# Kernel optimization log

Hardware: AMD Instinct MI355X
Metric: run time of the kernel (lower is better)

## Reference

```python
import jax, jax.numpy as jnp
import numpy as np

N_HEAD = 16
N_KV_HEAD = 4
HEAD_DIM = 128  # n_embd // n_head = 2048 // 16


def _apply_rope(x, pos, T):
    # x: [B, H, T, D]; RoPE cache built exactly like the torch module:
    # cos/sin use repeat_interleave(2) on freqs, rotation uses half-split.
    D = x.shape[-1]
    half = D // 2
    inv_freq = 1.0 / jnp.power(10000.0, jnp.arange(0, D, 2, dtype=jnp.float32) / D)  # [half]
    t = jnp.arange(pos, pos + T, dtype=jnp.float32)                                  # [T]
    freqs = t[:, None] * inv_freq[None, :]                                           # [T, half]
    freqs = jnp.repeat(freqs, 2, axis=-1)                                            # [T, D]
    cos = jnp.cos(freqs)[None, None, :, :]
    sin = jnp.sin(freqs)[None, None, :, :]
    x1, x2 = x[..., :half], x[..., half:]
    rotated = jnp.concatenate([-x2, x1], axis=-1)
    return x * cos + rotated * sin


def setup_inputs() -> dict:
    key = jax.random.key(0)
    ks = jax.random.split(key, 5)
    B, T, E = 2, 2048, 2048
    KV = N_KV_HEAD * HEAD_DIM  # 512
    s = 0.02
    return {
        "x": jax.random.normal(ks[0], (B, T, E), dtype=jnp.float32),
        "Wq": jax.random.normal(ks[1], (E, E), dtype=jnp.float32) * s,
        "Wk": jax.random.normal(ks[2], (E, KV), dtype=jnp.float32) * s,
        "Wv": jax.random.normal(ks[3], (E, KV), dtype=jnp.float32) * s,
        "Wproj": jax.random.normal(ks[4], (E, E), dtype=jnp.float32) * s,
        "pos": 0,
    }


def reference(x, Wq, Wk, Wv, Wproj, pos):
    B, T, E = x.shape
    H, HKV, D = N_HEAD, N_KV_HEAD, HEAD_DIM
    G = H // HKV  # query heads per kv head

    q = (x @ Wq).reshape(B, T, H, D).transpose(0, 2, 1, 3)     # [B,H,T,D]
    k = (x @ Wk).reshape(B, T, HKV, D).transpose(0, 2, 1, 3)   # [B,HKV,T,D]
    v = (x @ Wv).reshape(B, T, HKV, D).transpose(0, 2, 1, 3)   # [B,HKV,T,D]

    q = _apply_rope(q, pos, T)
    k = _apply_rope(k, pos, T)

    # GQA: group query heads over shared kv heads
    qg = q.reshape(B, HKV, G, T, D)
    scale = 1.0 / jnp.sqrt(jnp.asarray(D, dtype=x.dtype))
    scores = jnp.einsum('bkgtd,bksd->bkgts', qg, k) * scale    # [B,HKV,G,T,T]

    causal = jnp.tril(jnp.ones((T, T), dtype=bool))
    scores = jnp.where(causal, scores, jnp.finfo(scores.dtype).min)
    attn = jax.nn.softmax(scores, axis=-1)

    out = jnp.einsum('bkgts,bksd->bkgtd', attn, v)             # [B,HKV,G,T,D]
    y = out.reshape(B, H, T, D).transpose(0, 2, 1, 3).reshape(B, T, E)
    return y @ Wproj
```

## Files before the change

kernel.cpp:

```cpp
#include <hip/hip_runtime.h>
#include <hip/hip_bf16.h>
#include <stdint.h>

typedef unsigned short u16;
typedef float f32x4 __attribute__((ext_vector_type(4)));
typedef __bf16 bf16x8 __attribute__((ext_vector_type(8)));
typedef unsigned short u16x8 __attribute__((ext_vector_type(8)));
typedef float f32x4v __attribute__((ext_vector_type(4)));

#define T_SEQ 2048

__device__ __forceinline__ u16 f2bf(float f) {
    unsigned int u = __float_as_uint(f);
    unsigned int r = (u + 0x7fffu + ((u >> 16) & 1u)) >> 16;
    return (u16)r;
}
__device__ __forceinline__ float bf2f(u16 b) {
    return __uint_as_float(((unsigned int)b) << 16);
}

__device__ __forceinline__ void gload_lds16(const void* g, void* l) {
    __builtin_amdgcn_global_load_lds(
        (__attribute__((address_space(1))) void*)(g),
        (__attribute__((address_space(3))) void*)(l), 16, 0, 0);
}

__global__ void cast_f32_bf16(const float* __restrict__ in, u16* __restrict__ out, int n8) {
    int i = blockIdx.x * blockDim.x + threadIdx.x;
    if (i >= n8) return;
    const f32x4v* p = (const f32x4v*)(in + (size_t)i * 8);
    f32x4v a = p[0], b = p[1];
    u16x8 v;
    v[0]=f2bf(a.x); v[1]=f2bf(a.y); v[2]=f2bf(a.z); v[3]=f2bf(a.w);
    v[4]=f2bf(b.x); v[5]=f2bf(b.y); v[6]=f2bf(b.z); v[7]=f2bf(b.w);
    *(u16x8*)(out + (size_t)i * 8) = v;
}

__global__ void prep_w(const float* __restrict__ Wq, const float* __restrict__ Wk,
                       const float* __restrict__ Wv, const float* __restrict__ Wp,
                       u16* __restrict__ WtQKV, u16* __restrict__ WtP) {
    __shared__ alignas(16) float sW[64 * 68];
    const int t = threadIdx.x;
    const int y = blockIdx.y;
    const float* W; u16* dst; int N; int n0;
    if (y < 32)      { W = Wq; dst = WtQKV;                       N = 2048; n0 = y * 64; }
    else if (y < 40) { W = Wk; dst = WtQKV + (size_t)2048 * 2048; N = 512;  n0 = (y - 32) * 64; }
    else if (y < 48) { W = Wv; dst = WtQKV + (size_t)2560 * 2048; N = 512;  n0 = (y - 40) * 64; }
    else             { W = Wp; dst = WtP;                         N = 2048; n0 = (y - 48) * 64; }
    const int k0 = blockIdx.x * 64;
#pragma unroll
    for (int i = 0; i < 4; i++) {
        int kr = i * 16 + (t >> 4), nc = (t & 15) * 4;
        *(f32x4v*)&sW[kr * 68 + nc] = *(const f32x4v*)&W[(size_t)(k0 + kr) * N + n0 + nc];
    }
    __syncthreads();
#pragma unroll
    for (int i = 0; i < 2; i++) {
        int nr = i * 32 + (t >> 3), kc = (t & 7) * 8;
        u16x8 v;
#pragma unroll
        for (int j = 0; j < 8; j++) v[j] = f2bf(sW[(kc + j) * 68 + nr]);
        *(u16x8*)&dst[(size_t)(n0 + nr) * 2048 + k0 + kc] = v;
    }
}

__device__ __forceinline__ void stage_rows(const u16* g, u16* lds, int R, int kcol0, int K, int t) {
    int row = R + (t >> 3);
    int u = t & 7;
    gload_lds16(g + (size_t)row * K + kcol0 + ((u ^ (row & 7)) * 8), lds + row * 64 + u * 8);
}
__device__ __forceinline__ void stage_half256(const u16* g, u16* lds, int half, int j, int kcol0, int K, int t) {
    int idx = j * 512 + t;
    int group = idx >> 8;
    int r32 = (idx >> 3) & 31;
    int row = group * 64 + half * 32 + r32;
    int u = idx & 7;
    gload_lds16(g + (size_t)row * K + kcol0 + ((u ^ (row & 7)) * 8), lds + row * 64 + u * 8);
}
__device__ __forceinline__ bf16x8 lds_ld(const u16* lds, int row, int kc, int hl) {
    return *(const bf16x8*)&lds[row * 64 + (((kc * 4 + hl) ^ (row & 7)) * 8)];
}

__global__ __launch_bounds__(512, 2) void gemm_qkv(const u16* __restrict__ A, const u16* __restrict__ Bt,
                                                   u16* __restrict__ C, int M, int N, int K) {
    __shared__ alignas(16) u16 ldsA[2][256 * 64];
    __shared__ alignas(16) u16 ldsB[2][192 * 64];
    const int t = threadIdx.x, wave = t >> 6, lane = t & 63;
    const int l15 = lane & 15, hl = lane >> 4;
    const int wr = wave >> 2, wc = wave & 3;

    const int f = blockIdx.x;
    const int swz = (f & 7) * 32 + (f >> 3);
    const int bx = swz & 15, by = swz >> 4;
    const int m0 = bx * 256, n0 = by * 192;

    const u16* gA = A + (size_t)m0 * K;
    const u16* gB = Bt + (size_t)n0 * K;

    f32x4 acc[8][3];
    f32x4 z = {0.f, 0.f, 0.f, 0.f};
#pragma unroll
    for (int m = 0; m < 8; m++)
#pragma unroll
        for (int n = 0; n < 3; n++) acc[m][n] = z;

    stage_rows(gA, ldsA[0], 0, 0, K, t);
    stage_rows(gA, ldsA[0], 128, 0, K, t);
    stage_rows(gB, ldsB[0], 0, 0, K, t);
    stage_rows(gB, ldsB[0], 64, 0, K, t);
    stage_rows(gB, ldsB[0], 128, 0, K, t);
    stage_rows(gA, ldsA[0], 64, 0, K, t);
    stage_rows(gA, ldsA[0], 192, 0, K, t);

    const int KT = K >> 6;
    for (int kt = 0; kt < KT; ++kt) {
        const int c = kt & 1;
        const int kn = (kt + 1 < KT) ? (kt + 1) * 64 : kt * 64;
        const u16* lAc = ldsA[c];
        const u16* lBc = ldsB[c];
        u16* lAn = ldsA[c ^ 1];
        u16* lBn = ldsB[c ^ 1];

        bf16x8 aF[4][2], bF[3][2];

        asm volatile("s_waitcnt vmcnt(2)" ::: "memory");
        __builtin_amdgcn_s_barrier();
#pragma unroll
        for (int mi = 0; mi < 4; mi++)
#pragma unroll
            for (int kc = 0; kc < 2; kc++)
                aF[mi][kc] = lds_ld(lAc, wr * 128 + mi * 16 + l15, kc, hl);
#pragma unroll
        for (int n = 0; n < 3; n++)
#pragma unroll
            for (int kc = 0; kc < 2; kc++)
                bF[n][kc] = lds_ld(lBc, wc * 48 + n * 16 + l15, kc, hl);
        stage_rows(gA, lAn, 0, kn, K, t);
        stage_rows(gA, lAn, 128, kn, K, t);
        stage_rows(gB, lBn, 0, kn, K, t);
        __builtin_amdgcn_s_setprio(1);
#pragma unroll
        for (int mi = 0; mi < 4; mi++)
#pragma unroll
            for (int n = 0; n < 3; n++)
#pragma unroll
                for (int kc = 0; kc < 2; kc++)
                    acc[mi][n] = __builtin_amdgcn_mfma_f32_16x16x32_bf16(aF[mi][kc], bF[n][kc], acc[mi][n], 0, 0, 0);
        __builtin_amdgcn_s_setprio(0);

        asm volatile("s_waitcnt vmcnt(3)" ::: "memory");
        __builtin_amdgcn_s_barrier();
#pragma unroll
        for (int mi = 0; mi < 4; mi++)
#pragma unroll
            for (int kc = 0; kc < 2; kc++)
                aF[mi][kc] = lds_ld(lAc, wr * 128 + 64 + mi * 16 + l15, kc, hl);
        stage_rows(gB, lBn, 64, kn, K, t);
        stage_rows(gB, lBn, 128, kn, K, t);
        stage_rows(gA, lAn, 64, kn, K, t);
        stage_rows(gA, lAn, 192, kn, K, t);
        __builtin_amdgcn_s_setprio(1);
#pragma unroll
        for (int mi = 0; mi < 4; mi++)
#pragma unroll
            for (int n = 0; n < 3; n++)
#pragma unroll
                for (int kc = 0; kc < 2; kc++)
                    acc[4 + mi][n] = __builtin_amdgcn_mfma_f32_16x16x32_bf16(aF[mi][kc], bF[n][kc], acc[4 + mi][n], 0, 0, 0);
        __builtin_amdgcn_s_setprio(0);
    }

#pragma unroll
    for (int m = 0; m < 8; m++)
#pragma unroll
        for (int n = 0; n < 3; n++)
#pragma unroll
            for (int r = 0; r < 4; r++) {
                int row = m0 + wr * 128 + m * 16 + hl * 4 + r;
                int col = n0 + wc * 48 + n * 16 + l15;
                C[(size_t)row * N + col] = f2bf(acc[m][n][r]);
            }
}

__global__ __launch_bounds__(512, 2) void gemm_proj(const u16* __restrict__ A, const u16* __restrict__ Bt,
                                                    float* __restrict__ C, int M, int N, int K) {
    __shared__ alignas(16) u16 ldsA[2][128 * 64];
    __shared__ alignas(16) u16 ldsB[2][256 * 64];
    const int t = threadIdx.x, wave = t >> 6, lane = t & 63;
    const int l15 = lane & 15, hl = lane >> 4;
    const int wr = wave >> 2, wc = wave & 3;

    const int f = blockIdx.x;
    const int swz = (f & 7) * 32 + (f >> 3);
    const int bx = swz & 31, by = swz >> 5;
    const int m0 = bx * 128, n0 = by * 256;

    const u16* gA = A + (size_t)m0 * K;
    const u16* gB = Bt + (size_t)n0 * K;

    f32x4 acc[4][4];
    f32x4 z = {0.f, 0.f, 0.f, 0.f};
#pragma unroll
    for (int m = 0; m < 4; m++)
#pragma unroll
        for (int n = 0; n < 4; n++) acc[m][n] = z;

    stage_rows(gA, ldsA[0], 0, 0, K, t);
    stage_rows(gA, ldsA[0], 64, 0, K, t);
    stage_half256(gB, ldsB[0], 0, 0, 0, K, t);
    stage_half256(gB, ldsB[0], 0, 1, 0, K, t);
    stage_half256(gB, ldsB[0], 1, 0, 0, K, t);
    stage_half256(gB, ldsB[0], 1, 1, 0, K, t);

    const int KT = K >> 6;
    for (int kt = 0; kt < KT; ++kt) {
        const int c = kt & 1;
        const int kn = (kt + 1 < KT) ? (kt + 1) * 64 : kt * 64;
        const u16* lAc = ldsA[c];
        const u16* lBc = ldsB[c];
        u16* lAn = ldsA[c ^ 1];
        u16* lBn = ldsB[c ^ 1];

        bf16x8 aF[4][2], bF[2][2];

        asm volatile("s_waitcnt vmcnt(2)" ::: "memory");
        __builtin_amdgcn_s_barrier();
#pragma unroll
        for (int mi = 0; mi < 4; mi++)
#pragma unroll
            for (int kc = 0; kc < 2; kc++)
                aF[mi][kc] = lds_ld(lAc, wr * 64 + mi * 16 + l15, kc, hl);
#pragma unroll
        for (int n = 0; n < 2; n++)
#pragma unroll
            for (int kc = 0; kc < 2; kc++)
                bF[n][kc] = lds_ld(lBc, wc * 64 + n * 16 + l15, kc, hl);
        stage_rows(gA, lAn, 0, kn, K, t);
        stage_rows(gA, lAn, 64, kn, K, t);
        stage_half256(gB, lBn, 0, 0, kn, K, t);
        stage_half256(gB, lBn, 0, 1, kn, K, t);
        __builtin_amdgcn_s_setprio(1);
#pragma unroll
        for (int mi = 0; mi < 4; mi++)
#pragma unroll
            for (int n = 0; n < 2; n++)
#pragma unroll
                for (int kc = 0; kc < 2; kc++)
                    acc[mi][n] = __builtin_amdgcn_mfma_f32_16x16x32_bf16(aF[mi][kc], bF[n][kc], acc[mi][n], 0, 0, 0);
        __builtin_amdgcn_s_setprio(0);

        asm volatile("s_waitcnt vmcnt(4)" ::: "memory");
        __builtin_amdgcn_s_barrier();
#pragma unroll
        for (int n = 0; n < 2; n++)
#pragma unroll
            for (int kc = 0; kc < 2; kc++)
                bF[n][kc] = lds_ld(lBc, wc * 64 + 32 + n * 16 + l15, kc, hl);
        stage_half256(gB, lBn, 1, 0, kn, K, t);
        stage_half256(gB, lBn, 1, 1, kn, K, t);
        __builtin_amdgcn_s_setprio(1);
#pragma unroll
        for (int mi = 0; mi < 4; mi++)
#pragma unroll
            for (int n = 0; n < 2; n++)
#pragma unroll
                for (int kc = 0; kc < 2; kc++)
                    acc[mi][2 + n] = __builtin_amdgcn_mfma_f32_16x16x32_bf16(aF[mi][kc], bF[n][kc], acc[mi][2 + n], 0, 0, 0);
        __builtin_amdgcn_s_setprio(0);
    }

#pragma unroll
    for (int m = 0; m < 4; m++)
#pragma unroll
        for (int n = 0; n < 4; n++)
#pragma unroll
            for (int r = 0; r < 4; r++) {
                int row = m0 + wr * 64 + m * 16 + hl * 4 + r;
                int col = n0 + wc * 64 + n * 16 + l15;
                C[(size_t)row * N + col] = acc[m][n][r];
            }
}

__global__ void rope_vtrans(u16* __restrict__ qkv, u16* __restrict__ vt,
                            const int* __restrict__ pos) {
    __shared__ alignas(16) u16 sT[64 * 72];
    const int t = threadIdx.x;
    if (blockIdx.x < 512) {
        const int f = blockIdx.x;
        const int t0 = (f & 31) * 64;
        const int d0 = ((f >> 5) & 1) * 64;
        const int kh = (f >> 6) & 3, b = f >> 8;
#pragma unroll
        for (int i = 0; i < 2; i++) {
            int tr = i * 32 + (t >> 3), dc = (t & 7) * 8;
            *(u16x8*)&sT[tr * 72 + dc] =
                *(const u16x8*)&qkv[(size_t)(b * T_SEQ + t0 + tr) * 3072 + 2560 + kh * 128 + d0 + dc];
        }
        __syncthreads();
#pragma unroll
        for (int i = 0; i < 2; i++) {
            int dr = i * 32 + (t >> 3), tc = (t & 7) * 8;
            u16x8 v;
#pragma unroll
            for (int j = 0; j < 8; j++) v[j] = sT[(tc + j) * 72 + dr];
            *(u16x8*)&vt[((size_t)(b * 4 + kh) * 128 + d0 + dr) * 2048 + t0 + tc] = v;
        }
    } else {
        int tid = (blockIdx.x - 512) * 256 + t;
        int j = tid & 63;
        int rest = tid >> 6;
        int slice = rest % 20;
        int row = rest / 20;
        if (row >= 2 * T_SEQ) return;
        float tpos = (float)((row % T_SEQ) + pos[0]);
        int base = (slice < 16) ? slice * 128 : 2048 + (slice - 16) * 128;
        u16* p = qkv + (size_t)row * 3072 + base;
        float x1 = bf2f(p[j]), x2 = bf2f(p[j + 64]);
        const float c0 = 0.20762050593045702f;
        int i = j >> 1;
        float fA = tpos * exp2f(-(float)i * c0);
        float fB = tpos * exp2f(-(float)(32 + i) * c0);
        float o1 = x1 * cosf(fA) - x2 * sinf(fA);
        float o2 = x2 * cosf(fB) + x1 * sinf(fB);
        p[j] = f2bf(o1);
        p[j + 64] = f2bf(o2);
    }
}

__global__ __launch_bounds__(256, 2) void attn(const u16* __restrict__ qkv,
                                               const u16* __restrict__ vt,
                                               u16* __restrict__ out) {
    __shared__ alignas(16) u16 sK[2][8192];
    __shared__ alignas(16) u16 sV[8192];
    __shared__ alignas(16) u16 sP[4 * 32 * 72];
    const int t = threadIdx.x, wave = t >> 6, lane = t & 63;
    const int l15 = lane & 15, hl = lane >> 4;

    const int f = blockIdx.x;
    const int sel = f >> 8, u = f & 255;
    const int bkh = u & 7, b = bkh >> 2, kh = bkh & 3;
    const int h = kh * 4 + ((u >> 3) & 3);
    const int j = u >> 5;
    const int a = sel ? (15 - j) : j;
    const int q0 = a * 128;
    const int nt = 2 * a + 2;

    const float sc = 0.08838834764831845f;

    bf16x8 qf[2][4];
#pragma unroll
    for (int m = 0; m < 2; m++)
#pragma unroll
        for (int c = 0; c < 4; c++) {
            const u16* qp = qkv + (size_t)(b * T_SEQ + q0 + wave * 32 + m * 16 + l15) * 3072
                            + h * 128 + c * 32 + hl * 8;
            u16x8 raw = *(const u16x8*)qp;
            u16x8 sv_;
#pragma unroll
            for (int e = 0; e < 8; e++) sv_[e] = f2bf(bf2f(raw[e]) * sc);
            qf[m][c] = *(bf16x8*)&sv_;
        }

    u16x8 onesu;
#pragma unroll
    for (int e = 0; e < 8; e++) onesu[e] = 0x3F80;
    const bf16x8 onesf = *(bf16x8*)&onesu;

    float mrow[2][4];
    f32x4 o[2][8];
    f32x4 osum[2];
    f32x4 z = {0.f, 0.f, 0.f, 0.f};
#pragma unroll
    for (int m = 0; m < 2; m++) {
#pragma unroll
        for (int r = 0; r < 4; r++) mrow[m][r] = -1e30f;
        osum[m] = z;
#pragma unroll
        for (int n8 = 0; n8 < 8; n8++) o[m][n8] = z;
    }

    asm volatile("s_waitcnt vmcnt(0)" ::: "memory");

    const u16* kgbase = qkv + (size_t)(b * T_SEQ) * 3072 + 2048 + kh * 128;
    const u16* vgbase = vt + (size_t)(b * 4 + kh) * 128 * 2048;

#pragma unroll
    for (int p = 0; p < 4; p++) {
        int i = p * 256 + t;
        int row = i >> 4, c = i & 15;
        gload_lds16(kgbase + (size_t)row * 3072 + ((c ^ (row & 7)) * 8), (u16*)sK[0] + i * 8);
    }

    int cur = 0;
    for (int it = 0; it < nt; ++it) {
        const int kv0 = it * 64;
        const int kvn = (it + 1 < nt) ? kv0 + 64 : kv0;
#pragma unroll
        for (int p = 0; p < 4; p++) {
            int i = p * 256 + t;
            int row = i >> 3, c = i & 7;
            gload_lds16(vgbase + (size_t)row * 2048 + kv0 + ((c ^ (row & 7)) * 8), sV + i * 8);
        }
#pragma unroll
        for (int p = 0; p < 4; p++) {
            int i = p * 256 + t;
            int row = i >> 4, c = i & 15;
            gload_lds16(kgbase + (size_t)(kvn + row) * 3072 + ((c ^ (row & 7)) * 8),
                        (u16*)sK[cur ^ 1] + i * 8);
        }
        asm volatile("s_waitcnt vmcnt(8)" ::: "memory");
        __builtin_amdgcn_s_barrier();

        f32x4 sA[2][4];
#pragma unroll
        for (int m = 0; m < 2; m++)
#pragma unroll
            for (int n = 0; n < 4; n++) sA[m][n] = z;
#pragma unroll
        for (int n = 0; n < 4; n++)
#pragma unroll
            for (int c = 0; c < 4; c++) {
                int row = n * 16 + l15;
                bf16x8 kf = *(const bf16x8*)&sK[cur][row * 128 + (((c * 4 + hl) ^ (row & 7)) * 8)];
#pragma unroll
                for (int m = 0; m < 2; m++)
                    sA[m][n] = __builtin_amdgcn_mfma_f32_16x16x32_bf16(qf[m][c], kf, sA[m][n], 0, 0, 0);
            }

#pragma unroll
        for (int m = 0; m < 2; m++)
#pragma unroll
            for (int r = 0; r < 4; r++) {
                const int grow = q0 + wave * 32 + m * 16 + hl * 4 + r;
                float mv[4];
#pragma unroll
                for (int n = 0; n < 4; n++)
                    mv[n] = (kv0 + n * 16 + l15 <= grow) ? sA[m][n][r] : -1e30f;
                float pmax = fmaxf(fmaxf(mv[0], mv[1]), fmaxf(mv[2], mv[3]));
                if (__builtin_expect(__any(pmax > mrow[m][r] + 8.f), 0)) {
                    float mx = pmax;
#pragma unroll
                    for (int off = 1; off < 16; off <<= 1) mx = fmaxf(mx, __shfl_xor(mx, off));
                    float mnew = fmaxf(mrow[m][r], mx);
                    float alpha = __expf(mrow[m][r] - mnew);
                    mrow[m][r] = mnew;
#pragma unroll
                    for (int n8 = 0; n8 < 8; n8++) o[m][n8][r] *= alpha;
                    osum[m][r] *= alpha;
                }
#pragma unroll
                for (int n = 0; n < 4; n++)
                    sP[(wave * 32 + m * 16 + hl * 4 + r) * 72 + n * 16 + l15] =
                        f2bf(__expf(mv[n] - mrow[m][r]));
            }

        asm volatile("s_waitcnt vmcnt(4)" ::: "memory");
        __builtin_amdgcn_s_barrier();

        bf16x8 pa[2][2];
#pragma unroll
        for (int m = 0; m < 2; m++)
#pragma unroll
            for (int k2 = 0; k2 < 2; k2++)
                pa[m][k2] = *(const bf16x8*)&sP[(wave * 32 + m * 16 + l15) * 72 + k2 * 32 + hl * 8];
#pragma unroll
        for (int m = 0; m < 2; m++)
#pragma unroll
            for (int k2 = 0; k2 < 2; k2++)
                osum[m] = __builtin_amdgcn_mfma_f32_16x16x32_bf16(pa[m][k2], onesf, osum[m], 0, 0, 0);
#pragma unroll
        for (int n8 = 0; n8 < 8; n8++)
#pragma unroll
            for (int k2 = 0; k2 < 2; k2++) {
                int d = n8 * 16 + l15;
                bf16x8 vf = *(const bf16x8*)&sV[d * 64 + (((k2 * 4 + hl) ^ (d & 7)) * 8)];
#pragma unroll
                for (int m = 0; m < 2; m++)
                    o[m][n8] = __builtin_amdgcn_mfma_f32_16x16x32_bf16(pa[m][k2], vf, o[m][n8], 0, 0, 0);
            }
        __builtin_amdgcn_s_barrier();
        cur ^= 1;
    }

#pragma unroll
    for (int m = 0; m < 2; m++)
#pragma unroll
        for (int r = 0; r < 4; r++) {
            float inv = 1.f / osum[m][r];
            int orow = b * T_SEQ + q0 + wave * 32 + m * 16 + hl * 4 + r;
#pragma unroll
            for (int n8 = 0; n8 < 8; n8++)
                out[(size_t)orow * 2048 + h * 128 + n8 * 16 + l15] = f2bf(o[m][n8][r] * inv);
        }
}

extern "C" void kernel_launch(void* const* d_in, const int* in_sizes, int n_in,
                              void* d_out, int out_size, void* d_ws, size_t ws_size,
                              hipStream_t stream) {
    const float* x  = (const float*)d_in[0];
    const float* Wq = (const float*)d_in[1];
    const float* Wk = (const float*)d_in[2];
    const float* Wv = (const float*)d_in[3];
    const float* Wp = (const float*)d_in[4];
    const int*   pos = (const int*)d_in[5];

    char* ws = (char*)d_ws;
    u16* xbf   = (u16*)(ws);
    u16* WtQKV = (u16*)(ws + 16777216);
    u16* WtP   = (u16*)(ws + 29360128);
    u16* QKV   = (u16*)(ws + 37748736);
    u16* Vt    = (u16*)(ws + 62914560);
    u16* AO    = (u16*)(ws + 67108864);

    cast_f32_bf16<<<4096, 256, 0, stream>>>(x, xbf, 1048576);
    prep_w<<<dim3(32, 80), 256, 0, stream>>>(Wq, Wk, Wv, Wp, WtQKV, WtP);

    gemm_qkv<<<256, 512, 0, stream>>>(xbf, WtQKV, QKV, 4096, 3072, 2048);
    rope_vtrans<<<21504, 256, 0, stream>>>(QKV, Vt, pos);
    attn<<<512, 256, 0, stream>>>(QKV, Vt, AO);
    gemm_proj<<<256, 512, 0, stream>>>(AO, WtP, (float*)d_out, 4096, 2048, 2048);
}
```

Measured before the change: 202.4 us.

## Split attention work across 8 waves with 16 query rows each

The attention kernel now launches 512 threads per block. Each of the 8 waves handles 16 query rows instead of 32, which halves the per-wave accumulator and Q-fragment registers. Cooperative K/V loads are spread across more threads, and the launch bounds and waitcnt counts are adjusted to match. The goal is higher occupancy and better latency hiding, at the cost of less K/V fragment reuse per LDS read (each K/V fragment now feeds one MFMA instead of two) and more LDS traffic per unit of compute.

```diff
diff --git a/kernel.cpp b/kernel.cpp
--- a/kernel.cpp
+++ b/kernel.cpp
@@ -327,12 +327,12 @@
     }
 }
 
-__global__ __launch_bounds__(256, 2) void attn(const u16* __restrict__ qkv,
+__global__ __launch_bounds__(512, 4) void attn(const u16* __restrict__ qkv,
                                                const u16* __restrict__ vt,
                                                u16* __restrict__ out) {
     __shared__ alignas(16) u16 sK[2][8192];
     __shared__ alignas(16) u16 sV[8192];
-    __shared__ alignas(16) u16 sP[4 * 32 * 72];
+    __shared__ alignas(16) u16 sP[128 * 72];
     const int t = threadIdx.x, wave = t >> 6, lane = t & 63;
     const int l15 = lane & 15, hl = lane >> 4;
 
@@ -347,37 +347,32 @@
 
     const float sc = 0.08838834764831845f;
 
-    bf16x8 qf[2][4];
-#pragma unroll
-    for (int m = 0; m < 2; m++)
-#pragma unroll
-        for (int c = 0; c < 4; c++) {
-            const u16* qp = qkv + (size_t)(b * T_SEQ + q0 + wave * 32 + m * 16 + l15) * 3072
-                            + h * 128 + c * 32 + hl * 8;
-            u16x8 raw = *(const u16x8*)qp;
-            u16x8 sv_;
-#pragma unroll
-            for (int e = 0; e < 8; e++) sv_[e] = f2bf(bf2f(raw[e]) * sc);
-            qf[m][c] = *(bf16x8*)&sv_;
-        }
+    bf16x8 qf[4];
+#pragma unroll
+    for (int c = 0; c < 4; c++) {
+        const u16* qp = qkv + (size_t)(b * T_SEQ + q0 + wave * 16 + l15) * 3072
+                        + h * 128 + c * 32 + hl * 8;
+        u16x8 raw = *(const u16x8*)qp;
+        u16x8 sv_;
+#pragma unroll
+        for (int e = 0; e < 8; e++) sv_[e] = f2bf(bf2f(raw[e]) * sc);
+        qf[c] = *(bf16x8*)&sv_;
+    }
 
     u16x8 onesu;
 #pragma unroll
     for (int e = 0; e < 8; e++) onesu[e] = 0x3F80;
     const bf16x8 onesf = *(bf16x8*)&onesu;
 
-    float mrow[2][4];
-    f32x4 o[2][8];
-    f32x4 osum[2];
+    float mrow[4];
+    f32x4 o[8];
+    f32x4 osum;
     f32x4 z = {0.f, 0.f, 0.f, 0.f};
 #pragma unroll
-    for (int m = 0; m < 2; m++) {
-#pragma unroll
-        for (int r = 0; r < 4; r++) mrow[m][r] = -1e30f;
-        osum[m] = z;
-#pragma unroll
-        for (int n8 = 0; n8 < 8; n8++) o[m][n8] = z;
-    }
+    for (int r = 0; r < 4; r++) mrow[r] = -1e30f;
+    osum = z;
+#pragma unroll
+    for (int n8 = 0; n8 < 8; n8++) o[n8] = z;
 
     asm volatile("s_waitcnt vmcnt(0)" ::: "memory");
 
@@ -385,8 +380,8 @@
     const u16* vgbase = vt + (size_t)(b * 4 + kh) * 128 * 2048;
 
 #pragma unroll
-    for (int p = 0; p < 4; p++) {
-        int i = p * 256 + t;
+    for (int p = 0; p < 2; p++) {
+        int i = p * 512 + t;
         int row = i >> 4, c = i & 15;
         gload_lds16(kgbase + (size_t)row * 3072 + ((c ^ (row & 7)) * 8), (u16*)sK[0] + i * 8);
     }
@@ -396,102 +391,88 @@
         const int kv0 = it * 64;
         const int kvn = (it + 1 < nt) ? kv0 + 64 : kv0;
 #pragma unroll
-        for (int p = 0; p < 4; p++) {
-            int i = p * 256 + t;
+        for (int p = 0; p < 2; p++) {
+            int i = p * 512 + t;
             int row = i >> 3, c = i & 7;
             gload_lds16(vgbase + (size_t)row * 2048 + kv0 + ((c ^ (row & 7)) * 8), sV + i * 8);
         }
 #pragma unroll
-        for (int p = 0; p < 4; p++) {
-            int i = p * 256 + t;
+        for (int p = 0; p < 2; p++) {
+            int i = p * 512 + t;
             int row = i >> 4, c = i & 15;
             gload_lds16(kgbase + (size_t)(kvn + row) * 3072 + ((c ^ (row & 7)) * 8),
                         (u16*)sK[cur ^ 1] + i * 8);
         }
-        asm volatile("s_waitcnt vmcnt(8)" ::: "memory");
-        __builtin_amdgcn_s_barrier();
-
-        f32x4 sA[2][4];
-#pragma unroll
-        for (int m = 0; m < 2; m++)
-#pragma unroll
-            for (int n = 0; n < 4; n++) sA[m][n] = z;
+        asm volatile("s_waitcnt vmcnt(4)" ::: "memory");
+        __builtin_amdgcn_s_barrier();
+
+        f32x4 sA[4];
+#pragma unroll
+        for (int n = 0; n < 4; n++) sA[n] = z;
 #pragma unroll
         for (int n = 0; n < 4; n++)
 #pragma unroll
             for (int c = 0; c < 4; c++) {
                 int row = n * 16 + l15;
                 bf16x8 kf = *(const bf16x8*)&sK[cur][row * 128 + (((c * 4 + hl) ^ (row & 7)) * 8)];
-#pragma unroll
-                for (int m = 0; m < 2; m++)
-                    sA[m][n] = __builtin_amdgcn_mfma_f32_16x16x32_bf16(qf[m][c], kf, sA[m][n], 0, 0, 0);
+                sA[n] = __builtin_amdgcn_mfma_f32_16x16x32_bf16(qf[c], kf, sA[n], 0, 0, 0);
             }
 
 #pragma unroll
-        for (int m = 0; m < 2; m++)
-#pragma unroll
-            for (int r = 0; r < 4; r++) {
-                const int grow = q0 + wave * 32 + m * 16 + hl * 4 + r;
-                float mv[4];
-#pragma unroll
-                for (int n = 0; n < 4; n++)
-                    mv[n] = (kv0 + n * 16 + l15 <= grow) ? sA[m][n][r] : -1e30f;
-                float pmax = fmaxf(fmaxf(mv[0], mv[1]), fmaxf(mv[2], mv[3]));
-                if (__builtin_expect(__any(pmax > mrow[m][r] + 8.f), 0)) {
-                    float mx = pmax;
-#pragma unroll
-                    for (int off = 1; off < 16; off <<= 1) mx = fmaxf(mx, __shfl_xor(mx, off));
-                    float mnew = fmaxf(mrow[m][r], mx);
-                    float alpha = __expf(mrow[m][r] - mnew);
-                    mrow[m][r] = mnew;
-#pragma unroll
-                    for (int n8 = 0; n8 < 8; n8++) o[m][n8][r] *= alpha;
-                    osum[m][r] *= alpha;
-                }
-#pragma unroll
-                for (int n = 0; n < 4; n++)
-                    sP[(wave * 32 + m * 16 + hl * 4 + r) * 72 + n * 16 + l15] =
-                        f2bf(__expf(mv[n] - mrow[m][r]));
+        for (int r = 0; r < 4; r++) {
+            const int grow = q0 + wave * 16 + hl * 4 + r;
+            float mv[4];
+#pragma unroll
+            for (int n = 0; n < 4; n++)
+                mv[n] = (kv0 + n * 16 + l15 <= grow) ? sA[n][r] : -1e30f;
+            float pmax = fmaxf(fmaxf(mv[0], mv[1]), fmaxf(mv[2], mv[3]));
+            if (__builtin_expect(__any(pmax > mrow[r] + 8.f), 0)) {
+                float mx = pmax;
+#pragma unroll
+                for (int off = 1; off < 16; off <<= 1) mx = fmaxf(mx, __shfl_xor(mx, off));
+                float mnew = fmaxf(mrow[r], mx);
+                float alpha = __expf(mrow[r] - mnew);
+                mrow[r] = mnew;
+#pragma unroll
+                for (int n8 = 0; n8 < 8; n8++) o[n8][r] *= alpha;
+                osum[r] *= alpha;
             }
-
-        asm volatile("s_waitcnt vmcnt(4)" ::: "memory");
-        __builtin_amdgcn_s_barrier();
-
-        bf16x8 pa[2][2];
-#pragma unroll
-        for (int m = 0; m < 2; m++)
-#pragma unroll
-            for (int k2 = 0; k2 < 2; k2++)
-                pa[m][k2] = *(const bf16x8*)&sP[(wave * 32 + m * 16 + l15) * 72 + k2 * 32 + hl * 8];
-#pragma unroll
-        for (int m = 0; m < 2; m++)
-#pragma unroll
-            for (int k2 = 0; k2 < 2; k2++)
-                osum[m] = __builtin_amdgcn_mfma_f32_16x16x32_bf16(pa[m][k2], onesf, osum[m], 0, 0, 0);
+#pragma unroll
+            for (int n = 0; n < 4; n++)
+                sP[(wave * 16 + hl * 4 + r) * 72 + n * 16 + l15] =
+                    f2bf(__expf(mv[n] - mrow[r]));
+        }
+
+        asm volatile("s_waitcnt vmcnt(2)" ::: "memory");
+        __builtin_amdgcn_s_barrier();
+
+        bf16x8 pa[2];
+#pragma unroll
+        for (int k2 = 0; k2 < 2; k2++)
+            pa[k2] = *(const bf16x8*)&sP[(wave * 16 + l15) * 72 + k2 * 32 + hl * 8];
+#pragma unroll
+        for (int k2 = 0; k2 < 2; k2++)
+            osum = __builtin_amdgcn_mfma_f32_16x16x32_bf16(pa[k2], onesf, osum, 0, 0, 0);
 #pragma unroll
         for (int n8 = 0; n8 < 8; n8++)
 #pragma unroll
             for (int k2 = 0; k2 < 2; k2++) {
                 int d = n8 * 16 + l15;
                 bf16x8 vf = *(const bf16x8*)&sV[d * 64 + (((k2 * 4 + hl) ^ (d & 7)) * 8)];
-#pragma unroll
-                for (int m = 0; m < 2; m++)
-                    o[m][n8] = __builtin_amdgcn_mfma_f32_16x16x32_bf16(pa[m][k2], vf, o[m][n8], 0, 0, 0);
+                o[n8] = __builtin_amdgcn_mfma_f32_16x16x32_bf16(pa[k2], vf, o[n8], 0, 0, 0);
             }
         __builtin_amdgcn_s_barrier();
         cur ^= 1;
     }
 
 #pragma unroll
-    for (int m = 0; m < 2; m++)
-#pragma unroll
-        for (int r = 0; r < 4; r++) {
-            float inv = 1.f / osum[m][r];
-            int orow = b * T_SEQ + q0 + wave * 32 + m * 16 + hl * 4 + r;
-#pragma unroll
-            for (int n8 = 0; n8 < 8; n8++)
-                out[(size_t)orow * 2048 + h * 128 + n8 * 16 + l15] = f2bf(o[m][n8][r] * inv);
-        }
+    for (int r = 0; r < 4; r++) {
+        float inv = 1.f / osum[r];
+        int orow = b * T_SEQ + q0 + wave * 16 + hl * 4 + r;
+#pragma unroll
+        for (int n8 = 0; n8 < 8; n8++)
+            out[(size_t)orow * 2048 + h * 128 + n8 * 16 + l15] = f2bf(o[n8][r] * inv);
+    }
 }
 
 extern "C" void kernel_launch(void* const* d_in, const int* in_sizes, int n_in,
@@ -517,6 +498,6 @@
 
     gemm_qkv<<<256, 512, 0, stream>>>(xbf, WtQKV, QKV, 4096, 3072, 2048);
     rope_vtrans<<<21504, 256, 0, stream>>>(QKV, Vt, pos);
-    attn<<<512, 256, 0, stream>>>(QKV, Vt, AO);
+    attn<<<512, 512, 0, stream>>>(QKV, Vt, AO);
     gemm_proj<<<256, 512, 0, stream>>>(AO, WtP, (float*)d_out, 4096, 2048, 2048);
 }
```

New measurement: 191.6 us. 5.3% less time.
